# Performance work log

Hardware: AMD Instinct MI355X
Metric: run time of the kernel (lower is better)

## Reference

```python
import jax, jax.numpy as jnp
import numpy as np

N_NODES = 2048
EMBED = 256
STATE = 128
HID = 256
N_ACT = 256
TEAMS = 8
PAIR_F = 14


def setup_inputs() -> dict:
    key = jax.random.key(0)
    ks = jax.random.split(key, 12)
    B, T = 16, 32
    node_embeddings = jax.random.normal(ks[0], (N_NODES, EMBED), jnp.float32)
    states = jax.random.normal(ks[1], (B, T, STATE), jnp.float32)
    pair_features = jax.random.normal(ks[2], (B, T, N_ACT, PAIR_F), jnp.float32)
    proc_action_indices = jax.random.randint(ks[3], (N_ACT,), 0, N_NODES)
    in_dim = EMBED * 4 + PAIR_F
    s = lambda k, sh, fan: jax.random.normal(k, sh, jnp.float32) / np.sqrt(fan)
    return {
        "node_embeddings": node_embeddings,
        "states": states,
        "pair_features": pair_features,
        "proc_action_indices": proc_action_indices,
        "team_table": jax.random.normal(ks[4], (TEAMS, EMBED), jnp.float32),
        "Ws": s(ks[5], (STATE, EMBED), STATE),
        "bs": jnp.zeros((EMBED,), jnp.float32),
        "W1": s(ks[6], (in_dim, HID), in_dim),
        "b1": jnp.zeros((HID,), jnp.float32),
        "W2": s(ks[7], (HID, HID), HID),
        "b2": jnp.zeros((HID,), jnp.float32),
        "W3": s(ks[8], (HID, 1), HID),
        "b3": jnp.zeros((1,), jnp.float32),
    }


def reference(node_embeddings, states, pair_features, proc_action_indices,
              team_table, Ws, bs, W1, b1, W2, b2, W3, b3):
    B, T, A, F = pair_features.shape
    team_ids = jnp.arange(A) % TEAMS  # registered buffer
    # [A, E] gathered / per-action embeddings
    proc_emb = node_embeddings[proc_action_indices]          # [A, E]
    team_emb = team_table[team_ids]                          # [A, E]
    global_emb = jnp.mean(node_embeddings, axis=0)           # [E]
    state_emb = jax.nn.relu(states @ Ws + bs)                # [B, T, E]
    # broadcast + concat -> [B, T, A, 4E + F]
    bT = (B, T, A)
    scorer_input = jnp.concatenate([
        jnp.broadcast_to(proc_emb[None, None], bT + (proc_emb.shape[-1],)),
        jnp.broadcast_to(team_emb[None, None], bT + (team_emb.shape[-1],)),
        jnp.broadcast_to(global_emb[None, None, None], bT + (global_emb.shape[-1],)),
        jnp.broadcast_to(state_emb[:, :, None], bT + (state_emb.shape[-1],)),
        pair_features,
    ], axis=-1)
    h = jax.nn.relu(scorer_input @ W1 + b1)
    h = jax.nn.relu(h @ W2 + b2)
    scores = (h @ W3 + b3)[..., 0]  # [B, T, A]
    return scores[:, :, None, :]    # [B, T, 1, A]
```

## Files before the change

kernel.cpp:

```cpp
#include <hip/hip_runtime.h>
#include <hip/hip_bf16.h>

#define N_NODES 2048
#define EMBED 256
#define STATE 128
#define HID 256
#define N_ACT 256
#define TEAMS 8
#define PAIR_F 14
#define BT_TOTAL 512
#define M_TOTAL (BT_TOTAL * N_ACT)

typedef _Float16 f16_t;
typedef _Float16 f16x8 __attribute__((ext_vector_type(8)));
typedef _Float16 f16x4 __attribute__((ext_vector_type(4)));
typedef _Float16 f16x2 __attribute__((ext_vector_type(2)));
typedef float f32x4 __attribute__((ext_vector_type(4)));

__device__ __forceinline__ size_t par_idx(int a, int n) {
    return (size_t)(a >> 4) * 4096 + (size_t)(n >> 2) * 64 + (a & 15) * 4 + (n & 3);
}

__device__ __forceinline__ f16x8 gather8(const float* __restrict__ W, int k0, int n, int ld) {
    f16x8 r;
#pragma unroll
    for (int j = 0; j < 8; ++j) r[j] = (f16_t)W[(size_t)(k0 + j) * ld + n];
    return r;
}

__device__ __forceinline__ f16x2 pk_relu(f16x2 x) {
    f16x2 r;
    asm("v_pk_max_f16 %0, %1, %2" : "=v"(r) : "v"(x), "v"(f16x2{(_Float16)0, (_Float16)0}));
    return r;
}

__device__ __forceinline__ f16x2 cvt_pk(float lo, float hi) {
    return __builtin_bit_cast(f16x2, __builtin_amdgcn_cvt_pkrtz(lo, hi));
}

__global__ void k_prepA(const float* __restrict__ ne, const int* __restrict__ idx,
                        const float* __restrict__ team, const float* __restrict__ states,
                        const float* __restrict__ Ws, const float* __restrict__ W1,
                        float* __restrict__ gpart, f16_t* __restrict__ vecs,
                        f16_t* __restrict__ W1abT, f16_t* __restrict__ W1cT,
                        f16_t* __restrict__ W1dT, f16_t* __restrict__ WsT,
                        f16_t* __restrict__ states_h) {
    int bid = blockIdx.x;
    if (bid < 64) {
        int t = threadIdx.x;
        float s = 0.f;
        const float* base = ne + (size_t)bid * 32 * EMBED + t;
#pragma unroll
        for (int i = 0; i < 32; ++i) s += base[(size_t)i * EMBED];
        gpart[bid * EMBED + t] = s;
        return;
    }
    int u = (bid - 64) * 256 + threadIdx.x;
    if (u < 16384) {
        int a = u >> 6, e = (u & 63) * 8;
        f16x8 r;
        if (e < 256) {
            const float* src = ne + (size_t)idx[a] * EMBED + e;
#pragma unroll
            for (int j = 0; j < 8; ++j) r[j] = (f16_t)src[j];
        } else {
            const float* src = team + (size_t)(a % TEAMS) * EMBED + (e - 256);
#pragma unroll
            for (int j = 0; j < 8; ++j) r[j] = (f16_t)src[j];
        }
        *(f16x8*)(vecs + (size_t)u * 8) = r;
        return;
    }
    u -= 16384;
    if (u < 16384) {
        int c = u & 15, q = (u >> 4) & 3, kb = (u >> 6) & 15, g = u >> 10;
        *(f16x8*)(W1abT + (size_t)u * 8) = gather8(W1, kb * 32 + q * 8, g * 16 + c, HID);
        return;
    }
    u -= 16384;
    if (u < 8192) {
        int c = u & 15, q = (u >> 4) & 3, kb = (u >> 6) & 7, g = u >> 9;
        *(f16x8*)(W1cT + (size_t)u * 8) = gather8(W1, 512 + kb * 32 + q * 8, g * 16 + c, HID);
        return;
    }
    u -= 8192;
    if (u < 8192) {
        int c = u & 15, q = (u >> 4) & 3, kb = (u >> 6) & 7, g = u >> 9;
        *(f16x8*)(W1dT + (size_t)u * 8) = gather8(W1, 768 + kb * 32 + q * 8, g * 16 + c, HID);
        return;
    }
    u -= 8192;
    if (u < 4096) {
        int c = u & 15, q = (u >> 4) & 3, kb = (u >> 6) & 3, g = u >> 8;
        *(f16x8*)(WsT + (size_t)u * 8) = gather8(Ws, kb * 32 + q * 8, g * 16 + c, EMBED);
        return;
    }
    u -= 4096;
    if (u < 8192) {
        const float* src = states + (size_t)u * 8;
        f16x8 r;
#pragma unroll
        for (int j = 0; j < 8; ++j) r[j] = (f16_t)src[j];
        *(f16x8*)(states_h + (size_t)u * 8) = r;
    }
}

__global__ __launch_bounds__(256, 4) void k_prepB(
    const float* __restrict__ pf, const float* __restrict__ W1,
    const float* __restrict__ W2, const f16_t* __restrict__ states_h,
    const f16_t* __restrict__ WsT, const float* __restrict__ bs,
    const f16_t* __restrict__ W1dT, const f16_t* __restrict__ vecs,
    const f16_t* __restrict__ W1abT, const f16_t* __restrict__ W1cT,
    const float* __restrict__ gpart, const float* __restrict__ b1,
    f16_t* __restrict__ W2s, f16_t* __restrict__ w1pt,
    f16_t* __restrict__ paR, f16_t* __restrict__ pbt_h,
    f16_t* __restrict__ pf16) {
    __shared__ __align__(16) f16_t se[32 * 256];
    __shared__ __align__(16) f16_t gml[256];
    const int tid = threadIdx.x;
    const int wid = tid >> 6, lane = tid & 63;
    const int c = lane & 15, q = lane >> 4;
    int bid = blockIdx.x;

    if (bid < 48) {
        if (bid >= 16) {
            {
                float s = 0.f;
#pragma unroll 8
                for (int p = 0; p < 64; ++p) s += gpart[p * EMBED + tid];
                gml[tid] = (f16_t)(s * (1.0f / N_NODES));
            }
            __syncthreads();
            int b = bid - 16;
            const int m0 = (b >> 2) * 32, n0 = (b & 3) * 64;
            const int n = n0 + wid * 16 + c;
            const int g = n >> 4;
            f32x4 acc[2] = {f32x4{0, 0, 0, 0}, f32x4{0, 0, 0, 0}};
            for (int ks = 0; ks < 16; ++ks) {
                f16x8 bf = *(const f16x8*)(W1abT + (size_t)((g * 16 + ks) * 4 + q) * 128 + c * 8);
#pragma unroll
                for (int mi = 0; mi < 2; ++mi) {
                    f16x8 af = *(const f16x8*)(vecs + (size_t)(m0 + mi * 16 + c) * 512 + ks * 32 + q * 8);
                    acc[mi] = __builtin_amdgcn_mfma_f32_16x16x32_f16(af, bf, acc[mi], 0, 0, 0);
                }
            }
#pragma unroll
            for (int ks = 0; ks < 8; ++ks) {
                f16x8 bf = *(const f16x8*)(W1cT + (size_t)((g * 8 + ks) * 4 + q) * 128 + c * 8);
                f16x8 af = *(const f16x8*)(gml + ks * 32 + q * 8);
#pragma unroll
                for (int mi = 0; mi < 2; ++mi)
                    acc[mi] = __builtin_amdgcn_mfma_f32_16x16x32_f16(af, bf, acc[mi], 0, 0, 0);
            }
            float b1v = b1[n];
#pragma unroll
            for (int mi = 0; mi < 2; ++mi)
#pragma unroll
                for (int j = 0; j < 4; ++j) {
                    int a = m0 + mi * 16 + q * 4 + j;
                    paR[par_idx(a, n)] = (f16_t)(acc[mi][j] + b1v);
                }
            return;
        }

        const int bt0 = bid * 32;
        f32x4 acc[2][4];
#pragma unroll
        for (int mi = 0; mi < 2; ++mi)
#pragma unroll
            for (int ni = 0; ni < 4; ++ni) acc[mi][ni] = f32x4{0, 0, 0, 0};
#pragma unroll
        for (int ks = 0; ks < 4; ++ks) {
            f16x8 bh[4];
#pragma unroll
            for (int ni = 0; ni < 4; ++ni) {
                int g = wid * 4 + ni;
                bh[ni] = *(const f16x8*)(WsT + (size_t)((g * 4 + ks) * 4 + q) * 128 + c * 8);
            }
#pragma unroll
            for (int mi = 0; mi < 2; ++mi) {
                f16x8 af = *(const f16x8*)(states_h + (size_t)(bt0 + mi * 16 + c) * STATE + ks * 32 + q * 8);
#pragma unroll
                for (int ni = 0; ni < 4; ++ni)
                    acc[mi][ni] = __builtin_amdgcn_mfma_f32_16x16x32_f16(af, bh[ni], acc[mi][ni], 0, 0, 0);
            }
        }
#pragma unroll
        for (int mi = 0; mi < 2; ++mi)
#pragma unroll
            for (int ni = 0; ni < 4; ++ni) {
                float bsv = bs[wid * 64 + ni * 16 + c];
#pragma unroll
                for (int j = 0; j < 4; ++j) {
                    int m = mi * 16 + q * 4 + j;
                    int n = wid * 64 + ni * 16 + c;
                    se[m * 256 + (n ^ ((m & 7) << 3))] = (f16_t)fmaxf(acc[mi][ni][j] + bsv, 0.f);
                }
            }
#pragma unroll
        for (int mi = 0; mi < 2; ++mi)
#pragma unroll
            for (int ni = 0; ni < 4; ++ni) acc[mi][ni] = f32x4{0, 0, 0, 0};
        __syncthreads();
#pragma unroll
        for (int ks = 0; ks < 8; ++ks) {
            f16x8 bh[4];
#pragma unroll
            for (int ni = 0; ni < 4; ++ni) {
                int g = wid * 4 + ni;
                bh[ni] = *(const f16x8*)(W1dT + (size_t)((g * 8 + ks) * 4 + q) * 128 + c * 8);
            }
#pragma unroll
            for (int mi = 0; mi < 2; ++mi) {
                int m = mi * 16 + c;
                f16x8 ah = *(const f16x8*)(&se[m * 256 + ((ks * 32 + q * 8) ^ ((m & 7) << 3))]);
#pragma unroll
                for (int ni = 0; ni < 4; ++ni)
                    acc[mi][ni] = __builtin_amdgcn_mfma_f32_16x16x32_f16(ah, bh[ni], acc[mi][ni], 0, 0, 0);
            }
        }
#pragma unroll
        for (int mi = 0; mi < 2; ++mi)
#pragma unroll
            for (int ni = 0; ni < 4; ++ni)
#pragma unroll
                for (int j = 0; j < 4; ++j)
                    pbt_h[(size_t)(bt0 + mi * 16 + q * 4 + j) * HID + wid * 64 + ni * 16 + c] =
                        (f16_t)acc[mi][ni][j];
        return;
    }

    int u = (bid - 48) * 256 + tid;
    if (u < 262144) {
        int m = u >> 1, h = u & 1;
        const float* row = pf + (size_t)m * PAIR_F;
        f16x8 r;
        if (h == 0) {
#pragma unroll
            for (int j = 0; j < 4; ++j) {
                float2 v = *(const float2*)(row + j * 2);
                r[j * 2] = (f16_t)v.x; r[j * 2 + 1] = (f16_t)v.y;
            }
        } else {
#pragma unroll
            for (int j = 0; j < 3; ++j) {
                float2 v = *(const float2*)(row + 8 + j * 2);
                r[j * 2] = (f16_t)v.x; r[j * 2 + 1] = (f16_t)v.y;
            }
            r[6] = (f16_t)0.f; r[7] = (f16_t)0.f;
        }
        *(f16x8*)(pf16 + (size_t)u * 8) = r;
        return;
    }
    u -= 262144;
    if (u < 8192) {
        int c2 = u & 15, q2 = (u >> 4) & 3, kb = (u >> 6) & 7, g = u >> 9;
        *(f16x8*)(W2s + (size_t)u * 8) = gather8(W2, kb * 32 + q2 * 8, g * 16 + c2, HID);
        return;
    }
    u -= 8192;
    if (u < 1024) {
        int c2 = u & 15, q2 = (u >> 4) & 3, g = u >> 6;
        int n = g * 16 + c2, k0 = q2 * 8;
        f16x8 r;
#pragma unroll
        for (int j = 0; j < 8; ++j) {
            int k = k0 + j;
            r[j] = (f16_t)((k < PAIR_F) ? W1[(size_t)(1024 + k) * HID + n] : 0.f);
        }
        *(f16x8*)(w1pt + (size_t)u * 8) = r;
    }
}

__global__ __launch_bounds__(512, 4) void k_main(
    const f16_t* __restrict__ pf16, const f16_t* __restrict__ paR,
    const f16_t* __restrict__ pbt, const f16_t* __restrict__ w2s,
    const f16_t* __restrict__ w1pt, const float* __restrict__ b2,
    const float* __restrict__ W3, const float* __restrict__ b3,
    float* __restrict__ out) {
    __shared__ __align__(16) f16_t Ah[128 * 256];
    __shared__ float red[4][128];

    const int tid = threadIdx.x;
    const int wid = tid >> 6, lane = tid & 63;
    const int wr = wid >> 2, wc = wid & 3;
    const int c = lane & 15, q = lane >> 4;

    const int r0 = blockIdx.x * 128;
    const int bt = r0 >> 8;
    const int a0 = r0 & 255;

    f32x4 acc[16];
#pragma unroll
    for (int i = 0; i < 16; ++i) acc[i] = f32x4{0, 0, 0, 0};

    f16x4 pbtv[4];
#pragma unroll
    for (int nf = 0; nf < 4; ++nf)
        pbtv[nf] = *(const f16x4*)(pbt + (size_t)bt * HID + wc * 64 + nf * 16 + q * 4);

    f16x8 af[4];
#pragma unroll
    for (int nf = 0; nf < 4; ++nf) {
        int g = wc * 4 + nf;
        af[nf] = *(const f16x8*)(w1pt + (size_t)(g * 4 + q) * 128 + c * 8);
    }

    f16x4 pavA[4], pavB[4];
    {
        int n0 = wc * 64 + 0 * 16 + q * 4;
#pragma unroll
        for (int mf = 0; mf < 4; ++mf)
            pavA[mf] = *(const f16x4*)(paR + (size_t)((a0 >> 4) + wr * 4 + mf) * 4096 +
                                       (size_t)(n0 >> 2) * 64 + c * 4);
    }

#pragma unroll
    for (int mf = 0; mf < 4; ++mf) {
        int m = wr * 64 + mf * 16 + c;
        f16x8 bf;
        if (q < 2) bf = *(const f16x8*)(pf16 + (size_t)(r0 + m) * 16 + q * 8);
        else bf = f16x8{(_Float16)0, (_Float16)0, (_Float16)0, (_Float16)0,
                        (_Float16)0, (_Float16)0, (_Float16)0, (_Float16)0};
        __builtin_amdgcn_s_setprio(1);
#pragma unroll
        for (int nf = 0; nf < 4; ++nf)
            acc[nf * 4 + mf] = __builtin_amdgcn_mfma_f32_16x16x32_f16(af[nf], bf, acc[nf * 4 + mf], 0, 0, 0);
        __builtin_amdgcn_s_setprio(0);
    }

#pragma unroll
    for (int nf = 0; nf < 4; ++nf) {
        if (nf < 3) {
            int n1 = wc * 64 + (nf + 1) * 16 + q * 4;
#pragma unroll
            for (int mf = 0; mf < 4; ++mf)
                pavB[mf] = *(const f16x4*)(paR + (size_t)((a0 >> 4) + wr * 4 + mf) * 4096 +
                                           (size_t)(n1 >> 2) * 64 + c * 4);
        }
        int n0 = wc * 64 + nf * 16 + q * 4;
        f16x2 pb01 = {pbtv[nf][0], pbtv[nf][1]}, pb23 = {pbtv[nf][2], pbtv[nf][3]};
#pragma unroll
        for (int mf = 0; mf < 4; ++mf) {
            int m = wr * 64 + mf * 16 + c;
            f16x2 pa01 = {pavA[mf][0], pavA[mf][1]}, pa23 = {pavA[mf][2], pavA[mf][3]};
            f32x4 a = acc[nf * 4 + mf];
            f16x2 h01 = cvt_pk(a[0], a[1]);
            f16x2 h23 = cvt_pk(a[2], a[3]);
            h01 = pk_relu(h01 + pa01 + pb01);
            h23 = pk_relu(h23 + pa23 + pb23);
            f16x4 hv = __builtin_shufflevector(h01, h23, 0, 1, 2, 3);
            *(f16x4*)(&Ah[m * 256 + (n0 ^ ((m & 7) << 3))]) = hv;
        }
#pragma unroll
        for (int mf = 0; mf < 4; ++mf) pavA[mf] = pavB[mf];
    }

#pragma unroll
    for (int i = 0; i < 16; ++i) acc[i] = f32x4{0, 0, 0, 0};

    f16x8 bh[4];
#pragma unroll
    for (int ni = 0; ni < 4; ++ni) {
        int g = wc * 4 + ni;
        bh[ni] = *(const f16x8*)(w2s + (size_t)((g * 8 + 0) * 4 + q) * 128 + c * 8);
    }

    __syncthreads();

#pragma unroll
    for (int ks = 0; ks < 8; ++ks) {
        f16x8 bhn[4];
        if (ks < 7) {
#pragma unroll
            for (int ni = 0; ni < 4; ++ni) {
                int g = wc * 4 + ni;
                bhn[ni] = *(const f16x8*)(w2s + (size_t)((g * 8 + ks + 1) * 4 + q) * 128 + c * 8);
            }
        }
        f16x8 ahA, ahB;
        {
            int m = wr * 64 + 0 * 16 + c;
            ahA = *(const f16x8*)(&Ah[m * 256 + ((ks * 32 + q * 8) ^ ((m & 7) << 3))]);
        }
        __builtin_amdgcn_s_setprio(1);
#pragma unroll
        for (int mi = 0; mi < 4; ++mi) {
            if (mi < 3) {
                int m1 = wr * 64 + (mi + 1) * 16 + c;
                ahB = *(const f16x8*)(&Ah[m1 * 256 + ((ks * 32 + q * 8) ^ ((m1 & 7) << 3))]);
            }
#pragma unroll
            for (int ni = 0; ni < 4; ++ni)
                acc[mi * 4 + ni] = __builtin_amdgcn_mfma_f32_16x16x32_f16(ahA, bh[ni], acc[mi * 4 + ni], 0, 0, 0);
            ahA = ahB;
        }
        __builtin_amdgcn_s_setprio(0);
#pragma unroll
        for (int ni = 0; ni < 4; ++ni) bh[ni] = bhn[ni];
    }

    float p[4][4];
#pragma unroll
    for (int mi = 0; mi < 4; ++mi)
#pragma unroll
        for (int j = 0; j < 4; ++j) p[mi][j] = 0.f;
#pragma unroll
    for (int ni = 0; ni < 4; ++ni) {
        int n = wc * 64 + ni * 16 + c;
        float b2v = b2[n];
        float w3v = W3[n];
#pragma unroll
        for (int mi = 0; mi < 4; ++mi)
#pragma unroll
            for (int j = 0; j < 4; ++j)
                p[mi][j] = fmaf(fmaxf(acc[mi * 4 + ni][j] + b2v, 0.f), w3v, p[mi][j]);
    }
#pragma unroll
    for (int off = 1; off < 16; off <<= 1)
#pragma unroll
        for (int mi = 0; mi < 4; ++mi)
#pragma unroll
            for (int j = 0; j < 4; ++j) p[mi][j] += __shfl_xor(p[mi][j], off, 64);

    if (c == 0) {
#pragma unroll
        for (int mi = 0; mi < 4; ++mi)
#pragma unroll
            for (int j = 0; j < 4; ++j) red[wc][wr * 64 + mi * 16 + q * 4 + j] = p[mi][j];
    }
    __syncthreads();

    if (tid < 128) {
        out[(size_t)r0 + tid] = red[0][tid] + red[1][tid] + red[2][tid] + red[3][tid] + b3[0];
    }
}

extern "C" void kernel_launch(void* const* d_in, const int* in_sizes, int n_in,
                              void* d_out, int out_size, void* d_ws, size_t ws_size,
                              hipStream_t stream) {
    (void)in_sizes; (void)n_in; (void)out_size; (void)ws_size;
    const float* ne     = (const float*)d_in[0];
    const float* states = (const float*)d_in[1];
    const float* pf     = (const float*)d_in[2];
    const int*   idx    = (const int*)d_in[3];
    const float* team   = (const float*)d_in[4];
    const float* Ws     = (const float*)d_in[5];
    const float* bs     = (const float*)d_in[6];
    const float* W1     = (const float*)d_in[7];
    const float* b1     = (const float*)d_in[8];
    const float* W2     = (const float*)d_in[9];
    const float* b2     = (const float*)d_in[10];
    const float* W3     = (const float*)d_in[11];
    const float* b3     = (const float*)d_in[12];
    float* out = (float*)d_out;

    char* ws = (char*)d_ws;
    float* gpart    = (float*)(ws + 0);
    f16_t* vecs     = (f16_t*)(ws + 65536);
    f16_t* W1abT    = (f16_t*)(ws + 327680);
    f16_t* W1cT     = (f16_t*)(ws + 589824);
    f16_t* W1dT     = (f16_t*)(ws + 720896);
    f16_t* WsT      = (f16_t*)(ws + 851968);
    f16_t* W2s      = (f16_t*)(ws + 917504);
    f16_t* w1pt     = (f16_t*)(ws + 1048576);
    f16_t* states_h = (f16_t*)(ws + 1064960);
    f16_t* paR      = (f16_t*)(ws + 1196032);
    f16_t* pbt_h    = (f16_t*)(ws + 1327104);
    f16_t* pf16     = (f16_t*)(ws + 1589248);

    k_prepA<<<64 + 240, 256, 0, stream>>>(ne, idx, team, states, Ws, W1,
                                          gpart, vecs, W1abT, W1cT, W1dT, WsT, states_h);
    k_prepB<<<48 + 1060, 256, 0, stream>>>(pf, W1, W2, states_h, WsT, bs, W1dT,
                                           vecs, W1abT, W1cT, gpart, b1,
                                           W2s, w1pt, paR, pbt_h, pf16);
    k_main<<<M_TOTAL / 128, 512, 0, stream>>>(pf16, paR, pbt_h, W2s, w1pt, b2, W3, b3, out);
}
```

Measured before the change: 42.78 us.

## Fuse pair-feature fp16 conversion into main kernel and stagger layer-2 K order

Removes the prep pass that converted the pair features to a padded fp16 buffer; k_main now reads the fp32 rows directly and converts them in registers, so the 1024 extra prep blocks and the intermediate write and read of the padded copy disappear. Separately, each wave column starts its layer-2 K loop at a different offset and delays the barrier until the third step. The idea is that early steps read only the Ah columns this wave wrote itself, so the barrier wait overlaps with MFMA work. The risk is uncoalesced 56-byte-stride fp32 loads inside the main kernel, and the early K steps must really depend only on the wave's own writes.

After: 44.46 us. 1.04x slower.

```diff
diff --git a/kernel.cpp b/kernel.cpp
--- a/kernel.cpp
+++ b/kernel.cpp
@@ -106,15 +106,14 @@
 }
 
 __global__ __launch_bounds__(256, 4) void k_prepB(
-    const float* __restrict__ pf, const float* __restrict__ W1,
-    const float* __restrict__ W2, const f16_t* __restrict__ states_h,
-    const f16_t* __restrict__ WsT, const float* __restrict__ bs,
-    const f16_t* __restrict__ W1dT, const f16_t* __restrict__ vecs,
-    const f16_t* __restrict__ W1abT, const f16_t* __restrict__ W1cT,
-    const float* __restrict__ gpart, const float* __restrict__ b1,
-    f16_t* __restrict__ W2s, f16_t* __restrict__ w1pt,
-    f16_t* __restrict__ paR, f16_t* __restrict__ pbt_h,
-    f16_t* __restrict__ pf16) {
+    const float* __restrict__ W1, const float* __restrict__ W2,
+    const f16_t* __restrict__ states_h, const f16_t* __restrict__ WsT,
+    const float* __restrict__ bs, const f16_t* __restrict__ W1dT,
+    const f16_t* __restrict__ vecs, const f16_t* __restrict__ W1abT,
+    const f16_t* __restrict__ W1cT, const float* __restrict__ gpart,
+    const float* __restrict__ b1, f16_t* __restrict__ W2s,
+    f16_t* __restrict__ w1pt, f16_t* __restrict__ paR,
+    f16_t* __restrict__ pbt_h) {
     __shared__ __align__(16) f16_t se[32 * 256];
     __shared__ __align__(16) f16_t gml[256];
     const int tid = threadIdx.x;
@@ -231,28 +230,6 @@
     }
 
     int u = (bid - 48) * 256 + tid;
-    if (u < 262144) {
-        int m = u >> 1, h = u & 1;
-        const float* row = pf + (size_t)m * PAIR_F;
-        f16x8 r;
-        if (h == 0) {
-#pragma unroll
-            for (int j = 0; j < 4; ++j) {
-                float2 v = *(const float2*)(row + j * 2);
-                r[j * 2] = (f16_t)v.x; r[j * 2 + 1] = (f16_t)v.y;
-            }
-        } else {
-#pragma unroll
-            for (int j = 0; j < 3; ++j) {
-                float2 v = *(const float2*)(row + 8 + j * 2);
-                r[j * 2] = (f16_t)v.x; r[j * 2 + 1] = (f16_t)v.y;
-            }
-            r[6] = (f16_t)0.f; r[7] = (f16_t)0.f;
-        }
-        *(f16x8*)(pf16 + (size_t)u * 8) = r;
-        return;
-    }
-    u -= 262144;
     if (u < 8192) {
         int c2 = u & 15, q2 = (u >> 4) & 3, kb = (u >> 6) & 7, g = u >> 9;
         *(f16x8*)(W2s + (size_t)u * 8) = gather8(W2, kb * 32 + q2 * 8, g * 16 + c2, HID);
@@ -273,7 +250,7 @@
 }
 
 __global__ __launch_bounds__(512, 4) void k_main(
-    const f16_t* __restrict__ pf16, const f16_t* __restrict__ paR,
+    const float* __restrict__ pf, const f16_t* __restrict__ paR,
     const f16_t* __restrict__ pbt, const f16_t* __restrict__ w2s,
     const f16_t* __restrict__ w1pt, const float* __restrict__ b2,
     const float* __restrict__ W3, const float* __restrict__ b3,
@@ -318,10 +295,26 @@
 #pragma unroll
     for (int mf = 0; mf < 4; ++mf) {
         int m = wr * 64 + mf * 16 + c;
-        f16x8 bf;
-        if (q < 2) bf = *(const f16x8*)(pf16 + (size_t)(r0 + m) * 16 + q * 8);
-        else bf = f16x8{(_Float16)0, (_Float16)0, (_Float16)0, (_Float16)0,
-                        (_Float16)0, (_Float16)0, (_Float16)0, (_Float16)0};
+        const float* row = pf + (size_t)(r0 + m) * PAIR_F;
+        f16x8 bf = f16x8{(_Float16)0, (_Float16)0, (_Float16)0, (_Float16)0,
+                         (_Float16)0, (_Float16)0, (_Float16)0, (_Float16)0};
+        if (q == 0) {
+            float2 v0 = *(const float2*)(row);
+            float2 v1 = *(const float2*)(row + 2);
+            float2 v2 = *(const float2*)(row + 4);
+            float2 v3 = *(const float2*)(row + 6);
+            bf[0] = (f16_t)v0.x; bf[1] = (f16_t)v0.y;
+            bf[2] = (f16_t)v1.x; bf[3] = (f16_t)v1.y;
+            bf[4] = (f16_t)v2.x; bf[5] = (f16_t)v2.y;
+            bf[6] = (f16_t)v3.x; bf[7] = (f16_t)v3.y;
+        } else if (q == 1) {
+            float2 v0 = *(const float2*)(row + 8);
+            float2 v1 = *(const float2*)(row + 10);
+            float2 v2 = *(const float2*)(row + 12);
+            bf[0] = (f16_t)v0.x; bf[1] = (f16_t)v0.y;
+            bf[2] = (f16_t)v1.x; bf[3] = (f16_t)v1.y;
+            bf[4] = (f16_t)v2.x; bf[5] = (f16_t)v2.y;
+        }
         __builtin_amdgcn_s_setprio(1);
 #pragma unroll
         for (int nf = 0; nf < 4; ++nf)
@@ -359,23 +352,24 @@
 #pragma unroll
     for (int i = 0; i < 16; ++i) acc[i] = f32x4{0, 0, 0, 0};
 
+    const int ks0 = wc * 2;
     f16x8 bh[4];
 #pragma unroll
     for (int ni = 0; ni < 4; ++ni) {
         int g = wc * 4 + ni;
-        bh[ni] = *(const f16x8*)(w2s + (size_t)((g * 8 + 0) * 4 + q) * 128 + c * 8);
-    }
-
-    __syncthreads();
-
-#pragma unroll
-    for (int ks = 0; ks < 8; ++ks) {
+        bh[ni] = *(const f16x8*)(w2s + (size_t)((g * 8 + ks0) * 4 + q) * 128 + c * 8);
+    }
+#pragma unroll
+    for (int kk = 0; kk < 8; ++kk) {
+        if (kk == 2) __syncthreads();
+        const int ks = (ks0 + kk) & 7;
         f16x8 bhn[4];
-        if (ks < 7) {
+        if (kk < 7) {
+            int ksn = (ks0 + kk + 1) & 7;
 #pragma unroll
             for (int ni = 0; ni < 4; ++ni) {
                 int g = wc * 4 + ni;
-                bhn[ni] = *(const f16x8*)(w2s + (size_t)((g * 8 + ks + 1) * 4 + q) * 128 + c * 8);
+                bhn[ni] = *(const f16x8*)(w2s + (size_t)((g * 8 + ksn) * 4 + q) * 128 + c * 8);
             }
         }
         f16x8 ahA, ahB;
@@ -467,12 +461,11 @@
     f16_t* states_h = (f16_t*)(ws + 1064960);
     f16_t* paR      = (f16_t*)(ws + 1196032);
     f16_t* pbt_h    = (f16_t*)(ws + 1327104);
-    f16_t* pf16     = (f16_t*)(ws + 1589248);
 
     k_prepA<<<64 + 240, 256, 0, stream>>>(ne, idx, team, states, Ws, W1,
                                           gpart, vecs, W1abT, W1cT, W1dT, WsT, states_h);
-    k_prepB<<<48 + 1060, 256, 0, stream>>>(pf, W1, W2, states_h, WsT, bs, W1dT,
-                                           vecs, W1abT, W1cT, gpart, b1,
-                                           W2s, w1pt, paR, pbt_h, pf16);
-    k_main<<<M_TOTAL / 128, 512, 0, stream>>>(pf16, paR, pbt_h, W2s, w1pt, b2, W3, b3, out);
-}
+    k_prepB<<<48 + 36, 256, 0, stream>>>(W1, W2, states_h, WsT, bs, W1dT,
+                                         vecs, W1abT, W1cT, gpart, b1,
+                                         W2s, w1pt, paR, pbt_h);
+    k_main<<<M_TOTAL / 128, 512, 0, stream>>>(pf, paR, pbt_h, W2s, w1pt, b2, W3, b3, out);
+}
```
